# Performance work log

Hardware: AMD Instinct MI355X
Metric: run time of the kernel (lower is better)

## Reference

```python
import jax, jax.numpy as jnp
import numpy as np

B, S, D_IN, D_H = 2048, 256, 128, 256
C2 = 2.7193  # time-decay log offset from the original module


def setup_inputs() -> dict:
    key = jax.random.key(0)
    k0, k1, k2, k3 = jax.random.split(key, 4)
    inputs = jax.random.normal(k0, (B, S, D_IN), dtype=jnp.float32)
    # time must be increasing so intervals are positive (log(dt + 2.7193) valid)
    dt = jax.random.uniform(k1, (B, S), minval=0.1, maxval=5.0, dtype=jnp.float32)
    time = jnp.cumsum(dt, axis=1)
    Wi = jax.random.normal(k2, (D_IN, D_H), dtype=jnp.float32) / np.sqrt(D_IN).astype(np.float32)
    bi = jnp.zeros((D_H,), dtype=jnp.float32)
    Wh = jax.random.normal(k3, (D_H, D_H), dtype=jnp.float32) / np.sqrt(D_H).astype(np.float32)
    bh = jnp.zeros((D_H,), dtype=jnp.float32)
    return {"inputs": inputs, "time": time, "Wi": Wi, "bi": bi, "Wh": Wh, "bh": bh}


def reference(inputs, time, Wi, bi, Wh, bh):
    Bsz, Slen, _ = inputs.shape
    H = Wh.shape[0]
    # time points -> intervals, then decay weight 1/log(dt + c2)
    dt = time[:, 1:] - time[:, :-1]                     # [B, S-1]
    w = 1.0 / jnp.log(dt + C2)                          # [B, S-1]
    # precompute all input projections once (original recomputes per gate)
    x_proj = jnp.einsum('bsd,dh->bsh', inputs[:, :-1], Wi) + bi  # [B, S-1, H]

    def step(carry, xs):
        h, c, o = carry
        xz, wt = xs                                     # xz:[B,H], wt:[B]
        z = xz + h @ Wh + bh                            # shared gate pre-activation
        g = jax.nn.sigmoid(z)                           # f_t == i_t == o_t (same linears in source)
        C_bar = jnp.tanh(z)
        C_S = jnp.tanh(c @ Wh + bh)                     # short-term memory
        C_star = (c - C_S) + C_S * wt[:, None]          # long-term + discounted short-term
        c_new = g * C_star + g * C_bar
        h_new = g * jnp.tanh(C_bar)
        return (h_new, c_new, g), None

    zeros = jnp.zeros((Bsz, H), dtype=inputs.dtype)
    (h, c, o), _ = jax.lax.scan(
        step, (zeros, zeros, zeros),
        (jnp.swapaxes(x_proj, 0, 1), w.T),
    )
    res = o @ Wh + bh                                   # linear_hidden(o_t) of last step
    return jnp.stack((res, h, c))                       # [3, B, H]
```

## Files before the change

### kernel.cpp

```cpp
#include <hip/hip_runtime.h>

typedef __attribute__((ext_vector_type(8))) short short8;
typedef __attribute__((ext_vector_type(4))) float floatx4;
typedef __attribute__((ext_vector_type(2))) float floatx2;
typedef __attribute__((ext_vector_type(2))) unsigned uintx2;

#define LOG2E 1.44269504088896340736f

#define BAR() asm volatile("s_waitcnt lgkmcnt(0)\n\ts_barrier" ::: "memory")

__device__ __forceinline__ floatx2 F2(float v) { return (floatx2){v, v}; }

__device__ __forceinline__ unsigned short f2bf(float f) {
  unsigned u = __float_as_uint(f);
  u += 0x7FFFu + ((u >> 16) & 1u);
  return (unsigned short)(u >> 16);
}

__device__ __forceinline__ unsigned cvtpk(float lo, float hi) {
  unsigned r;
  asm("v_cvt_pk_bf16_f32 %0, %1, %2" : "=v"(r) : "v"(lo), "v"(hi));
  return r;
}

__global__ __launch_bounds__(512, 1) void tlstm_kernel(
    const float* __restrict__ x, const float* __restrict__ tim,
    const float* __restrict__ Wi, const float* __restrict__ bi,
    const float* __restrict__ Wh, const float* __restrict__ bh,
    float* __restrict__ out)
{
  __shared__ __align__(16) unsigned short Sst[2 * 4352];
  __shared__ __align__(16) unsigned short Sx[2 * 2176];
  __shared__ __align__(16) float WMt[2048];

  const int tid = threadIdx.x;
  const int wv  = tid >> 6;
  const int l   = tid & 63;
  const int q   = l >> 4;
  const int r   = l & 15;
  const int b0  = blockIdx.x * 8;

  const int col1 = wv * 32 + r;
  const int col2 = col1 + 16;

  short8 wh[2][8];
#pragma unroll
  for (int tx = 0; tx < 2; ++tx)
#pragma unroll
    for (int c = 0; c < 8; ++c)
#pragma unroll
      for (int j = 0; j < 8; ++j)
        wh[tx][c][j] = (short)f2bf(Wh[(c * 32 + q * 8 + j) * 256 + wv * 32 + tx * 16 + r]);
  short8 wi[2][4];
#pragma unroll
  for (int tx = 0; tx < 2; ++tx)
#pragma unroll
    for (int c = 0; c < 4; ++c)
#pragma unroll
      for (int j = 0; j < 8; ++j)
        wi[tx][c][j] = (short)f2bf(Wi[(c * 32 + q * 8 + j) * 256 + wv * 32 + tx * 16 + r]);
  const float bh1 = bh[col1], bh2 = bh[col2];
  const float bi1 = bi[col1], bi2 = bi[col2];

  const int raS = r * 272 + ((q * 8) ^ (((r >> 2) & 3) << 3));
  const int raX = r * 136 + q * 8;
  const int iA1 = (4 * q) * 272 + (col1 ^ (q << 3));
  const int iA2 = (4 * q) * 272 + (col2 ^ (q << 3));
  const int xw  = (2 * wv + (l >> 5)) * 136 + 4 * (l & 31);
  const float* xbase = x + (long)(b0 + wv) * 32768 + (l >> 5) * 128 + 4 * (l & 31);

  {
    unsigned* S32 = (unsigned*)Sst;
    for (int i = tid; i < 2176; i += 512) S32[i] = 0;
  }
  for (int i = tid; i < 2040; i += 512) {
    int t = i >> 3, bl = i & 7;
    float t0 = tim[(b0 + bl) * 256 + t];
    float t1 = tim[(b0 + bl) * 256 + t + 1];
    WMt[i] = 1.f - 1.f / logf(t1 - t0 + 2.7193f);
  }
  {
    floatx4 v = *(const floatx4*)xbase;
    uintx2 pk = {cvtpk(v.x, v.y), cvtpk(v.z, v.w)};
    *(uintx2*)&Sx[xw] = pk;
  }
  __syncthreads();

  floatx2 cP0 = F2(0.f), cP1 = F2(0.f);
  floatx2 hP0 = F2(0.f), hP1 = F2(0.f);
  floatx2 gP0 = F2(0.f), gP1 = F2(0.f);
  int xro = 0;

  auto proc2 = [&](floatx2 zin, floatx2 cpin, floatx2& cio, floatx2& gio,
                   floatx2& hio, float wmv, int ih0, int ih1, int woff) {
    floatx2 z  = __builtin_elementwise_min(__builtin_elementwise_max(zin,  F2(-10.f)), F2(10.f));
    floatx2 cp = __builtin_elementwise_min(__builtin_elementwise_max(cpin, F2(-10.f)), F2(10.f));
    floatx2 mz = z * F2(-LOG2E);
    floatx2 u  = {__builtin_amdgcn_exp2f(mz.x), __builtin_amdgcn_exp2f(mz.y)};
    floatx2 u2 = u * u;
    floatx2 mc = cp * F2(-2.f * LOG2E);
    floatx2 v  = {__builtin_amdgcn_exp2f(mc.x), __builtin_amdgcn_exp2f(mc.y)};
    floatx2 a1 = u + F2(1.f), a2 = u2 + F2(1.f), a3 = v + F2(1.f);
    floatx2 p12 = a1 * a2;
    floatx2 pr  = p12 * a3;
    floatx2 D   = {__builtin_amdgcn_rcpf(pr.x), __builtin_amdgcn_rcpf(pr.y)};
    floatx2 Da3 = D * a3;
    floatx2 g   = Da3 * a2;
    floatx2 ir2 = Da3 * a1;
    floatx2 ir3 = D * p12;
    floatx2 Cb  = ir2 - u2 * ir2;
    floatx2 Cs  = ir3 - v * ir3;
    floatx2 Cst = cio - Cs * F2(wmv);
    floatx2 cn  = g * (Cst + Cb);
    floatx2 s   = Cb * Cb;
    floatx2 P   = F2(0.003592028f);
    P = P * s + F2(-0.008863236f);
    P = P * s + F2(0.021869488f);
    P = P * s + F2(-0.053968254f);
    P = P * s + F2(0.133333333f);
    P = P * s + F2(-0.333333333f);
    P = P * s + F2(1.0f);
    floatx2 hn = g * (Cb * P);
    unsigned pk0 = cvtpk(hn.x, cn.x);
    unsigned pk1 = cvtpk(hn.y, cn.y);
    Sst[woff + ih0]       = (unsigned short)pk0;
    Sst[woff + ih0 + 272] = (unsigned short)(pk0 >> 16);
    Sst[woff + ih1]       = (unsigned short)pk1;
    Sst[woff + ih1 + 272] = (unsigned short)(pk1 >> 16);
    cio = cn; gio = g; hio = hn;
  };

  floatx4 xa1, xa2;
  auto loadx = [&]() {
    short8 xf[4];
#pragma unroll
    for (int c = 0; c < 4; ++c)
      xf[c] = *(const short8*)&Sx[xro + raX + 32 * c];
    floatx4 x1 = {bi1, bi1, bi1, bi1};
    floatx4 x2 = {bi2, bi2, bi2, bi2};
#pragma unroll
    for (int c = 0; c < 4; ++c) {
      x1 = __builtin_amdgcn_mfma_f32_16x16x32_bf16(xf[c], wi[0][c], x1, 0, 0, 0);
      x2 = __builtin_amdgcn_mfma_f32_16x16x32_bf16(xf[c], wi[1][c], x2, 0, 0, 0);
    }
    xa1 = x1; xa2 = x2;
  };

  auto dostep = [&](int roff, int woff, int par, int wmoff) {
    short8 sf[8];
#pragma unroll
    for (int c = 0; c < 8; ++c)
      sf[c] = *(const short8*)&Sst[roff + raS + 32 * c];
    floatx4 a1e = {bh1, bh1, bh1, bh1}, a1o = {0.f, 0.f, 0.f, 0.f};
    floatx4 a2e = {bh2, bh2, bh2, bh2}, a2o = {0.f, 0.f, 0.f, 0.f};
#pragma unroll
    for (int c = 0; c < 8; c += 2) {
      a1e = __builtin_amdgcn_mfma_f32_16x16x32_bf16(sf[c],     wh[0][c],     a1e, 0, 0, 0);
      a1o = __builtin_amdgcn_mfma_f32_16x16x32_bf16(sf[c + 1], wh[0][c + 1], a1o, 0, 0, 0);
      a2e = __builtin_amdgcn_mfma_f32_16x16x32_bf16(sf[c],     wh[1][c],     a2e, 0, 0, 0);
      a2o = __builtin_amdgcn_mfma_f32_16x16x32_bf16(sf[c + 1], wh[1][c + 1], a2o, 0, 0, 0);
    }
    floatx4 A1 = a1e + a1o;
    floatx4 A2 = a2e + a2o;
    floatx2 wm = *(const floatx2*)&WMt[wmoff];
    floatx2 z0  = {A1[0] + xa1[par],     A2[0] + xa2[par]};
    floatx2 cp0 = {A1[1],                A2[1]};
    floatx2 z1  = {A1[2] + xa1[2 + par], A2[2] + xa2[2 + par]};
    floatx2 cp1 = {A1[3],                A2[3]};
    proc2(z0, cp0, cP0, gP0, hP0, wm.x, iA1,       iA2,       woff);
    proc2(z1, cp1, cP1, gP1, hP1, wm.y, iA1 + 544, iA2 + 544, woff);
    BAR();
  };

  for (int p = 0; p < 127; ++p) {
    floatx4 nv = *(const floatx4*)(xbase + (p + 1) * 256);
    loadx();
    dostep(0, 4352, 0, 16 * p + 2 * q);
    {
      uintx2 pk = {cvtpk(nv.x, nv.y), cvtpk(nv.z, nv.w)};
      *(uintx2*)&Sx[(xro ^ 2176) + xw] = pk;
    }
    dostep(4352, 0, 1, 16 * p + 8 + 2 * q);
    xro ^= 2176;
  }

  loadx();
  dostep(0, 4352, 0, 16 * 127 + 2 * q);

  Sst[iA1]       = f2bf(gP0.x);  Sst[iA1 + 272] = 0;
  Sst[iA1 + 544] = f2bf(gP1.x);  Sst[iA1 + 816] = 0;
  Sst[iA2]       = f2bf(gP0.y);  Sst[iA2 + 272] = 0;
  Sst[iA2 + 544] = f2bf(gP1.y);  Sst[iA2 + 816] = 0;
  BAR();
  short8 gf[8];
#pragma unroll
  for (int c = 0; c < 8; ++c)
    gf[c] = *(const short8*)&Sst[raS + 32 * c];
  floatx4 r1 = {bh1, bh1, bh1, bh1};
  floatx4 r2 = {bh2, bh2, bh2, bh2};
#pragma unroll
  for (int c = 0; c < 8; ++c) {
    r1 = __builtin_amdgcn_mfma_f32_16x16x32_bf16(gf[c], wh[0][c], r1, 0, 0, 0);
    r2 = __builtin_amdgcn_mfma_f32_16x16x32_bf16(gf[c], wh[1][c], r2, 0, 0, 0);
  }

  const long P  = 2048L * 256;
  const long o0 = (long)(b0 + 2 * q) * 256;
  const long o1 = o0 + 256;
  out[o0 + col1]         = r1[0];
  out[o1 + col1]         = r1[2];
  out[o0 + col2]         = r2[0];
  out[o1 + col2]         = r2[2];
  out[P + o0 + col1]     = hP0.x;
  out[P + o1 + col1]     = hP1.x;
  out[P + o0 + col2]     = hP0.y;
  out[P + o1 + col2]     = hP1.y;
  out[2 * P + o0 + col1] = cP0.x;
  out[2 * P + o1 + col1] = cP1.x;
  out[2 * P + o0 + col2] = cP0.y;
  out[2 * P + o1 + col2] = cP1.y;
}

extern "C" void kernel_launch(void* const* d_in, const int* in_sizes, int n_in,
                              void* d_out, int out_size, void* d_ws, size_t ws_size,
                              hipStream_t stream) {
  const float* xin = (const float*)d_in[0];
  const float* tim = (const float*)d_in[1];
  const float* Wi  = (const float*)d_in[2];
  const float* bi  = (const float*)d_in[3];
  const float* Wh  = (const float*)d_in[4];
  const float* bh  = (const float*)d_in[5];
  tlstm_kernel<<<dim3(256), dim3(512), 0, stream>>>(xin, tim, Wi, bi, Wh, bh, (float*)d_out);
}
```

Measured before the change: 248.4 us.

## Fold -log2e into weights, simplify clamps, and unroll x double-buffer loop

Pre-scales Wh, Wi and both biases by -log2(e) so the MFMA outputs are already in exp2 domain. This removes the per-element multiplies and turns the two-sided clamp into a single min, and the final linear output is rescaled by -ln2. It also drops the highest-order tanh polynomial term and uses single serial MFMA accumulator chains instead of even/odd split chains. The main loop is unrolled by two so the x double-buffer offsets become compile-time constants. The bf16 rounding of the scaled weights and the shorter polynomial slightly change numerics, and the serial MFMA chains lengthen dependency latency.

Result: faster. 238.7 us (-3.9%).

```diff
diff --git a/kernel.cpp b/kernel.cpp
--- a/kernel.cpp
+++ b/kernel.cpp
@@ -5,7 +5,9 @@
 typedef __attribute__((ext_vector_type(2))) float floatx2;
 typedef __attribute__((ext_vector_type(2))) unsigned uintx2;
 
-#define LOG2E 1.44269504088896340736f
+#define NLOG2E -1.44269504088896340736f
+#define NLN2   -0.69314718055994530942f
+#define CLMP    14.4269504089f
 
 #define BAR() asm volatile("s_waitcnt lgkmcnt(0)\n\ts_barrier" ::: "memory")
 
@@ -50,7 +52,7 @@
     for (int c = 0; c < 8; ++c)
 #pragma unroll
       for (int j = 0; j < 8; ++j)
-        wh[tx][c][j] = (short)f2bf(Wh[(c * 32 + q * 8 + j) * 256 + wv * 32 + tx * 16 + r]);
+        wh[tx][c][j] = (short)f2bf(NLOG2E * Wh[(c * 32 + q * 8 + j) * 256 + wv * 32 + tx * 16 + r]);
   short8 wi[2][4];
 #pragma unroll
   for (int tx = 0; tx < 2; ++tx)
@@ -58,9 +60,9 @@
     for (int c = 0; c < 4; ++c)
 #pragma unroll
       for (int j = 0; j < 8; ++j)
-        wi[tx][c][j] = (short)f2bf(Wi[(c * 32 + q * 8 + j) * 256 + wv * 32 + tx * 16 + r]);
-  const float bh1 = bh[col1], bh2 = bh[col2];
-  const float bi1 = bi[col1], bi2 = bi[col2];
+        wi[tx][c][j] = (short)f2bf(NLOG2E * Wi[(c * 32 + q * 8 + j) * 256 + wv * 32 + tx * 16 + r]);
+  const float bh1 = NLOG2E * bh[col1], bh2 = NLOG2E * bh[col2];
+  const float bi1 = NLOG2E * bi[col1], bi2 = NLOG2E * bi[col2];
 
   const int raS = r * 272 + ((q * 8) ^ (((r >> 2) & 3) << 3));
   const int raX = r * 136 + q * 8;
@@ -89,17 +91,15 @@
   floatx2 cP0 = F2(0.f), cP1 = F2(0.f);
   floatx2 hP0 = F2(0.f), hP1 = F2(0.f);
   floatx2 gP0 = F2(0.f), gP1 = F2(0.f);
-  int xro = 0;
 
   auto proc2 = [&](floatx2 zin, floatx2 cpin, floatx2& cio, floatx2& gio,
                    floatx2& hio, float wmv, int ih0, int ih1, int woff) {
-    floatx2 z  = __builtin_elementwise_min(__builtin_elementwise_max(zin,  F2(-10.f)), F2(10.f));
-    floatx2 cp = __builtin_elementwise_min(__builtin_elementwise_max(cpin, F2(-10.f)), F2(10.f));
-    floatx2 mz = z * F2(-LOG2E);
-    floatx2 u  = {__builtin_amdgcn_exp2f(mz.x), __builtin_amdgcn_exp2f(mz.y)};
+    floatx2 z  = __builtin_elementwise_min(zin,  F2(CLMP));
+    floatx2 cp = __builtin_elementwise_min(cpin, F2(CLMP));
+    floatx2 u  = {__builtin_amdgcn_exp2f(z.x), __builtin_amdgcn_exp2f(z.y)};
     floatx2 u2 = u * u;
-    floatx2 mc = cp * F2(-2.f * LOG2E);
-    floatx2 v  = {__builtin_amdgcn_exp2f(mc.x), __builtin_amdgcn_exp2f(mc.y)};
+    floatx2 c2 = cp + cp;
+    floatx2 v  = {__builtin_amdgcn_exp2f(c2.x), __builtin_amdgcn_exp2f(c2.y)};
     floatx2 a1 = u + F2(1.f), a2 = u2 + F2(1.f), a3 = v + F2(1.f);
     floatx2 p12 = a1 * a2;
     floatx2 pr  = p12 * a3;
@@ -113,8 +113,7 @@
     floatx2 Cst = cio - Cs * F2(wmv);
     floatx2 cn  = g * (Cst + Cb);
     floatx2 s   = Cb * Cb;
-    floatx2 P   = F2(0.003592028f);
-    P = P * s + F2(-0.008863236f);
+    floatx2 P   = F2(-0.008863236f);
     P = P * s + F2(0.021869488f);
     P = P * s + F2(-0.053968254f);
     P = P * s + F2(0.133333333f);
@@ -131,11 +130,11 @@
   };
 
   floatx4 xa1, xa2;
-  auto loadx = [&]() {
+  auto loadx = [&](int xoff) {
     short8 xf[4];
 #pragma unroll
     for (int c = 0; c < 4; ++c)
-      xf[c] = *(const short8*)&Sx[xro + raX + 32 * c];
+      xf[c] = *(const short8*)&Sx[xoff + raX + 32 * c];
     floatx4 x1 = {bi1, bi1, bi1, bi1};
     floatx4 x2 = {bi2, bi2, bi2, bi2};
 #pragma unroll
@@ -151,40 +150,53 @@
 #pragma unroll
     for (int c = 0; c < 8; ++c)
       sf[c] = *(const short8*)&Sst[roff + raS + 32 * c];
-    floatx4 a1e = {bh1, bh1, bh1, bh1}, a1o = {0.f, 0.f, 0.f, 0.f};
-    floatx4 a2e = {bh2, bh2, bh2, bh2}, a2o = {0.f, 0.f, 0.f, 0.f};
-#pragma unroll
-    for (int c = 0; c < 8; c += 2) {
-      a1e = __builtin_amdgcn_mfma_f32_16x16x32_bf16(sf[c],     wh[0][c],     a1e, 0, 0, 0);
-      a1o = __builtin_amdgcn_mfma_f32_16x16x32_bf16(sf[c + 1], wh[0][c + 1], a1o, 0, 0, 0);
-      a2e = __builtin_amdgcn_mfma_f32_16x16x32_bf16(sf[c],     wh[1][c],     a2e, 0, 0, 0);
-      a2o = __builtin_amdgcn_mfma_f32_16x16x32_bf16(sf[c + 1], wh[1][c + 1], a2o, 0, 0, 0);
-    }
-    floatx4 A1 = a1e + a1o;
-    floatx4 A2 = a2e + a2o;
+    floatx4 a1 = {bh1, bh1, bh1, bh1};
+#pragma unroll
+    for (int c = 0; c < 8; ++c)
+      a1 = __builtin_amdgcn_mfma_f32_16x16x32_bf16(sf[c], wh[0][c], a1, 0, 0, 0);
+    floatx4 a2 = {bh2, bh2, bh2, bh2};
+#pragma unroll
+    for (int c = 0; c < 8; ++c)
+      a2 = __builtin_amdgcn_mfma_f32_16x16x32_bf16(sf[c], wh[1][c], a2, 0, 0, 0);
     floatx2 wm = *(const floatx2*)&WMt[wmoff];
-    floatx2 z0  = {A1[0] + xa1[par],     A2[0] + xa2[par]};
-    floatx2 cp0 = {A1[1],                A2[1]};
-    floatx2 z1  = {A1[2] + xa1[2 + par], A2[2] + xa2[2 + par]};
-    floatx2 cp1 = {A1[3],                A2[3]};
+    floatx2 z0  = {a1[0] + xa1[par],     a2[0] + xa2[par]};
+    floatx2 cp0 = {a1[1],                a2[1]};
+    floatx2 z1  = {a1[2] + xa1[2 + par], a2[2] + xa2[2 + par]};
+    floatx2 cp1 = {a1[3],                a2[3]};
     proc2(z0, cp0, cP0, gP0, hP0, wm.x, iA1,       iA2,       woff);
     proc2(z1, cp1, cP1, gP1, hP1, wm.y, iA1 + 544, iA2 + 544, woff);
     BAR();
   };
 
-  for (int p = 0; p < 127; ++p) {
-    floatx4 nv = *(const floatx4*)(xbase + (p + 1) * 256);
-    loadx();
-    dostep(0, 4352, 0, 16 * p + 2 * q);
+  auto stage = [&](floatx4 nv, int xoff) {
+    uintx2 pk = {cvtpk(nv.x, nv.y), cvtpk(nv.z, nv.w)};
+    *(uintx2*)&Sx[xoff + xw] = pk;
+  };
+
+  for (int p = 0; p < 126; p += 2) {
     {
-      uintx2 pk = {cvtpk(nv.x, nv.y), cvtpk(nv.z, nv.w)};
-      *(uintx2*)&Sx[(xro ^ 2176) + xw] = pk;
+      floatx4 nv = *(const floatx4*)(xbase + (long)(p + 1) * 256);
+      loadx(0);
+      dostep(0, 4352, 0, 16 * p + 2 * q);
+      stage(nv, 2176);
+      dostep(4352, 0, 1, 16 * p + 8 + 2 * q);
     }
-    dostep(4352, 0, 1, 16 * p + 8 + 2 * q);
-    xro ^= 2176;
-  }
-
-  loadx();
+    {
+      floatx4 nv = *(const floatx4*)(xbase + (long)(p + 2) * 256);
+      loadx(2176);
+      dostep(0, 4352, 0, 16 * (p + 1) + 2 * q);
+      stage(nv, 0);
+      dostep(4352, 0, 1, 16 * (p + 1) + 8 + 2 * q);
+    }
+  }
+  {
+    floatx4 nv = *(const floatx4*)(xbase + (long)127 * 256);
+    loadx(0);
+    dostep(0, 4352, 0, 16 * 126 + 2 * q);
+    stage(nv, 2176);
+    dostep(4352, 0, 1, 16 * 126 + 8 + 2 * q);
+  }
+  loadx(2176);
   dostep(0, 4352, 0, 16 * 127 + 2 * q);
 
   Sst[iA1]       = f2bf(gP0.x);  Sst[iA1 + 272] = 0;
@@ -207,10 +219,10 @@
   const long P  = 2048L * 256;
   const long o0 = (long)(b0 + 2 * q) * 256;
   const long o1 = o0 + 256;
-  out[o0 + col1]         = r1[0];
-  out[o1 + col1]         = r1[2];
-  out[o0 + col2]         = r2[0];
-  out[o1 + col2]         = r2[2];
+  out[o0 + col1]         = NLN2 * r1[0];
+  out[o1 + col1]         = NLN2 * r1[2];
+  out[o0 + col2]         = NLN2 * r2[0];
+  out[o1 + col2]         = NLN2 * r2[2];
   out[P + o0 + col1]     = hP0.x;
   out[P + o1 + col1]     = hP1.x;
   out[P + o0 + col2]     = hP0.y;
```
